# Kernel optimization log

Hardware: AMD Instinct MI355X
Metric: run time of the kernel (lower is better)

The kernel has to match this reference:

```python
import jax, jax.numpy as jnp
import numpy as np

EPS = 1e-6

def rms_norm(x):
    return x * jax.lax.rsqrt(jnp.mean(x * x, axis=-1, keepdims=True) + EPS)

def setup_inputs() -> dict:
    key = jax.random.key(0)
    k_x, k_w = jax.random.split(key)
    T, B, D = 2048, 16, 1024
    x = jax.random.normal(k_x, (T, B, D), dtype=jnp.float32)
    h0 = jnp.zeros((B, D), dtype=jnp.float32)
    # xavier_uniform for W: limit = sqrt(6/(fan_in+fan_out)) = sqrt(6/(2D))
    limit = float(np.sqrt(6.0 / (2 * D)))
    W = jax.random.uniform(k_w, (D, D), dtype=jnp.float32, minval=-limit, maxval=limit)
    b = jnp.zeros((D,), dtype=jnp.float32)
    log_alpha = jnp.asarray(np.log(0.1), dtype=jnp.float32)
    return {"x": x, "h0": h0, "W": W, "b": b, "log_alpha": log_alpha}

def reference(x, h0, W, b, log_alpha):
    # x: [T,B,D], h0: [B,D], W: [D,D], b: [D], log_alpha: []
    alpha = jnp.exp(log_alpha)
    # Precompute all input projections in one big GEMM: [T,B,D]
    Wx_all = jnp.einsum('tbd,ed->tbe', x, W) + b

    def step(h, wx):
        h_new = rms_norm(h + alpha * wx)
        out = h_new * jax.nn.silu(h_new)
        return h_new, (h_new, out)

    _, (hs, outs) = jax.lax.scan(step, h0, Wx_all)
    h = jnp.concatenate([h0[None], hs], axis=0)  # [T+1,B,D]
    return outs, h
```

## Files before the change

### kernel.cpp

```cpp
#include <hip/hip_runtime.h>
#include <hip/hip_bf16.h>

#define T_STEPS 2048
#define BATCH 16
#define DIM 1024
#define EPSV 1e-6f
#define INVD (1.0f / 1024.0f)
#define SLOTF (BATCH * DIM)
#define SLOT4C (BATCH * DIM / 4)

typedef short short8 __attribute__((ext_vector_type(8)));
typedef float f32x4 __attribute__((ext_vector_type(4)));

struct alignas(16) bf16x8pack { __hip_bfloat16 v[8]; };

__global__ __launch_bounds__(256) void cvt_kernel(const float* __restrict__ src,
                                                  bf16x8pack* __restrict__ dst, int n8) {
  int i = blockIdx.x * blockDim.x + threadIdx.x;
  if (i >= n8) return;
  const float4* s4 = (const float4*)src + (size_t)i * 2;
  float4 a = s4[0];
  float4 b = s4[1];
  bf16x8pack p;
  p.v[0] = __float2bfloat16(a.x); p.v[1] = __float2bfloat16(a.y);
  p.v[2] = __float2bfloat16(a.z); p.v[3] = __float2bfloat16(a.w);
  p.v[4] = __float2bfloat16(b.x); p.v[5] = __float2bfloat16(b.y);
  p.v[6] = __float2bfloat16(b.z); p.v[7] = __float2bfloat16(b.w);
  dst[i] = p;
}

__global__ __launch_bounds__(256) void gemm_kernel(
    const __hip_bfloat16* __restrict__ Xb,
    const __hip_bfloat16* __restrict__ Wb,
    const float* __restrict__ bias,
    const float* __restrict__ log_alpha_p,
    float* __restrict__ hreg) {
  __shared__ __hip_bfloat16 As[128 * 32];
  __shared__ __hip_bfloat16 Bs[128 * 32];
  const int tid = threadIdx.x;
  const int wave = tid >> 6, lane = tid & 63;
  const int m0 = blockIdx.y * 128;
  const int e0 = blockIdx.x * 128;
  const int wm = (wave >> 1) * 64;
  const int wn = (wave & 1) * 64;
  const int l15 = lane & 15, l4 = lane >> 4;

  f32x4 acc[4][4] = {};

  const int srow = wave * 16 + (lane >> 2);
  const int sch = (lane & 3) * 8;

  for (int kt = 0; kt < DIM; kt += 32) {
    __syncthreads();
#pragma unroll
    for (int i = 0; i < 2; ++i) {
      const __hip_bfloat16* ga = Xb + (size_t)(m0 + i * 64 + srow) * DIM + kt + sch;
      const __hip_bfloat16* gb = Wb + (size_t)(e0 + i * 64 + srow) * DIM + kt + sch;
      __builtin_amdgcn_global_load_lds(
          (const __attribute__((address_space(1))) void*)ga,
          (__attribute__((address_space(3))) void*)((char*)As + (i * 64 + wave * 16) * 64),
          16, 0, 0);
      __builtin_amdgcn_global_load_lds(
          (const __attribute__((address_space(1))) void*)gb,
          (__attribute__((address_space(3))) void*)((char*)Bs + (i * 64 + wave * 16) * 64),
          16, 0, 0);
    }
    __syncthreads();
    short8 a[4], b[4];
#pragma unroll
    for (int f = 0; f < 4; ++f)
      a[f] = *(const short8*)((const char*)As + ((wm + f * 16 + l15) * 32 + l4 * 8) * 2);
#pragma unroll
    for (int g = 0; g < 4; ++g)
      b[g] = *(const short8*)((const char*)Bs + ((wn + g * 16 + l15) * 32 + l4 * 8) * 2);
#pragma unroll
    for (int f = 0; f < 4; ++f)
#pragma unroll
      for (int g = 0; g < 4; ++g)
        acc[f][g] = __builtin_amdgcn_mfma_f32_16x16x32_bf16(a[f], b[g], acc[f][g], 0, 0, 0);
  }
  const float alpha = __expf(log_alpha_p[0]);
#pragma unroll
  for (int g = 0; g < 4; ++g) {
    const int e = e0 + wn + g * 16 + l15;
    const float bv = bias[e];
#pragma unroll
    for (int f = 0; f < 4; ++f) {
#pragma unroll
      for (int r = 0; r < 4; ++r) {
        const int m = m0 + wm + f * 16 + l4 * 4 + r;
        hreg[(size_t)(m + BATCH) * DIM + e] = alpha * (acc[f][g][r] + bv);
      }
    }
  }
}

__device__ __forceinline__ float dpp_sum_reg(float x) {
  float acc = x;
#define DPP_ADD(ctrl)                                                              \
  {                                                                                \
    int t_ = __builtin_amdgcn_update_dpp(0, __float_as_int(acc), (ctrl), 0xf, 0xf, \
                                         true);                                    \
    acc += __int_as_float(t_);                                                     \
  }
  DPP_ADD(0x111); DPP_ADD(0x112); DPP_ADD(0x114); DPP_ADD(0x118);
  DPP_ADD(0x142); DPP_ADD(0x143);
#undef DPP_ADD
  return acc;
}

__global__ __launch_bounds__(64) void dots_kernel(const float* __restrict__ hreg,
                                                  float4* __restrict__ scal4) {
  const int t = blockIdx.x >> 4;
  const int b = blockIdx.x & 15;
  const int lane = threadIdx.x;
  const float4* w  = (const float4*)(hreg + (size_t)(t + 1) * SLOTF + b * DIM);
  const float4* m1 = (const float4*)(hreg + (size_t)(t    ) * SLOTF + b * DIM);
  const float4* m2 = (const float4*)(hreg + (size_t)(t - 1) * SLOTF + b * DIM);
  const float4* m3 = (const float4*)(hreg + (size_t)(t - 2) * SLOTF + b * DIM);
  float e = 0.f, d = 0.f, d2 = 0.f, d3 = 0.f;
#pragma unroll
  for (int j = 0; j < 4; ++j) {
    float4 a = w[lane + 64 * j];
    e = fmaf(a.x, a.x, fmaf(a.y, a.y, fmaf(a.z, a.z, fmaf(a.w, a.w, e))));
    if (t >= 1) {
      float4 p = m1[lane + 64 * j];
      d = fmaf(p.x, a.x, fmaf(p.y, a.y, fmaf(p.z, a.z, fmaf(p.w, a.w, d))));
    }
    if (t >= 2) {
      float4 p = m2[lane + 64 * j];
      d2 = fmaf(p.x, a.x, fmaf(p.y, a.y, fmaf(p.z, a.z, fmaf(p.w, a.w, d2))));
    }
    if (t >= 3) {
      float4 p = m3[lane + 64 * j];
      d3 = fmaf(p.x, a.x, fmaf(p.y, a.y, fmaf(p.z, a.z, fmaf(p.w, a.w, d3))));
    }
  }
  e = dpp_sum_reg(e);
  d = dpp_sum_reg(d);
  d2 = dpp_sum_reg(d2);
  d3 = dpp_sum_reg(d3);
  if (lane == 63) scal4[b * T_STEPS + t] = make_float4(e, d, d2, d3);
}

__global__ __launch_bounds__(256) void scan_kernel(
    const float* __restrict__ h0,
    const float4* __restrict__ scal4,
    float* __restrict__ hreg) {
  const int b = blockIdx.x;
  const int tid = threadIdx.x;
  const int wave = tid >> 6;
  const int lane = tid & 63;
  float4* h4 = (float4*)hreg;
  const int idx4 = b * 256 + tid;

  __shared__ float4 scLDS[T_STEPS];
  __shared__ float Gp[4][4];
  __shared__ float initP[4][8];

#pragma unroll
  for (int p = 0; p < 8; ++p)
    scLDS[p * 256 + tid] = scal4[b * T_STEPS + p * 256 + tid];

  float4 w[8];
  w[2] = h4[(size_t)SLOT4C * 3 + idx4];
  w[3] = h4[(size_t)SLOT4C * 4 + idx4];
  w[4] = h4[(size_t)SLOT4C * 5 + idx4];
  w[5] = h4[(size_t)SLOT4C * 6 + idx4];
  w[6] = h4[(size_t)SLOT4C * 7 + idx4];
  w[7] = h4[(size_t)SLOT4C * 8 + idx4];
  w[0] = h4[(size_t)SLOT4C * 9 + idx4];
  w[1] = h4[(size_t)SLOT4C * 10 + idx4];
  float4 w0v = h4[(size_t)SLOT4C * 1 + idx4];
  float4 w1v = h4[(size_t)SLOT4C * 2 + idx4];
  float4 h0v = ((const float4*)h0)[idx4];
  h4[idx4] = h0v;

  float4 s;
  s.x = h0v.x + w0v.x; s.y = h0v.y + w0v.y;
  s.z = h0v.z + w0v.z; s.w = h0v.w + w0v.w;
  float q  = fmaf(s.x, s.x, fmaf(s.y, s.y, fmaf(s.z, s.z, s.w * s.w)));
  float r  = fmaf(s.x, w1v.x, fmaf(s.y, w1v.y, fmaf(s.z, w1v.z, s.w * w1v.w)));
  float u2 = fmaf(s.x, w[2].x, fmaf(s.y, w[2].y, fmaf(s.z, w[2].z, s.w * w[2].w)));
  float g3 = fmaf(h0v.x, w[3].x, fmaf(h0v.y, w[3].y, fmaf(h0v.z, w[3].z, h0v.w * w[3].w)));
  float u4 = fmaf(s.x, w[4].x, fmaf(s.y, w[4].y, fmaf(s.z, w[4].z, s.w * w[4].w)));
  q = dpp_sum_reg(q); r = dpp_sum_reg(r); u2 = dpp_sum_reg(u2);
  g3 = dpp_sum_reg(g3); u4 = dpp_sum_reg(u4);
  if (lane == 63) {
    initP[wave][0] = q; initP[wave][1] = r; initP[wave][2] = u2;
    initP[wave][3] = g3; initP[wave][4] = u4;
  }
  __syncthreads();
  const float n1  = initP[0][0] + initP[1][0] + initP[2][0] + initP[3][0];
  const float b1  = initP[0][1] + initP[1][1] + initP[2][1] + initP[3][1];
  const float c2  = initP[0][2] + initP[1][2] + initP[2][2] + initP[3][2];
  const float G3v = initP[0][3] + initP[1][3] + initP[2][3] + initP[3][3];
  const float c4  = initP[0][4] + initP[1][4] + initP[2][4] + initP[3][4];

  float4 sc0 = scLDS[2];
  float4 sc1 = scLDS[3];
  const float e1 = scLDS[1].x;

  const float rinv1 = rsqrtf(fmaf(n1, INVD, EPSV));
  float n = fmaf(rinv1, fmaf(rinv1, n1, 2.0f * b1), e1);
  const float b2p = fmaf(rinv1, c2, sc0.y);
  float gr1 = G3v;
  float gr0 = rinv1 * c4;

  {
    float4 hv;
    hv.x = rinv1 * s.x; hv.y = rinv1 * s.y; hv.z = rinv1 * s.z; hv.w = rinv1 * s.w;
    h4[(size_t)SLOT4C * 1 + idx4] = hv;
    s.x = hv.x + w1v.x; s.y = hv.y + w1v.y; s.z = hv.z + w1v.z; s.w = hv.w + w1v.w;
  }
  float rm1 = rinv1, rm2 = 0.0f;

#define STEP(IEXPR, WS, W3S, SCA, GPW, GPR, GRW, GRU, MODE)                          \
  {                                                                                  \
    const int i_ = (IEXPR);                                                          \
    const float rinv = rsqrtf(fmaf(n, INVD, EPSV));                                  \
    float bb;                                                                        \
    if ((MODE) == 1) bb = b2p;                                                       \
    else bb = fmaf(rm1, fmaf(rm2, SCA.w + GRU, SCA.z), SCA.y);                       \
    n = fmaf(rinv, fmaf(rinv, n, 2.0f * bb), SCA.x);                                 \
    float4 hv_;                                                                      \
    hv_.x = rinv * s.x; hv_.y = rinv * s.y;                                          \
    hv_.z = rinv * s.z; hv_.w = rinv * s.w;                                          \
    h4[(size_t)SLOT4C * i_ + idx4] = hv_;                                            \
    s.x = hv_.x + w[WS].x; s.y = hv_.y + w[WS].y;                                    \
    s.z = hv_.z + w[WS].z; s.w = hv_.w + w[WS].w;                                    \
    float p_ = fmaf(hv_.x, w[W3S].x, fmaf(hv_.y, w[W3S].y,                           \
               fmaf(hv_.z, w[W3S].z, hv_.w * w[W3S].w)));                            \
    p_ = dpp_sum_reg(p_);                                                            \
    if (lane == 63) Gp[GPW][wave] = p_;                                              \
    if ((MODE) == 0) {                                                               \
      float4 g4_ = *(const float4*)&Gp[GPR][0];                                      \
      GRW = (g4_.x + g4_.y) + (g4_.z + g4_.w);                                       \
    }                                                                                \
    const int ipf_ = (i_ + 8 < T_STEPS) ? i_ + 8 : T_STEPS - 1;                      \
    w[WS] = h4[(size_t)SLOT4C * (ipf_ + 1) + idx4];                                  \
    const int isc_ = (i_ + 2 < T_STEPS) ? i_ + 2 : T_STEPS - 1;                      \
    SCA = scLDS[isc_];                                                               \
    rm2 = rm1; rm1 = rinv;                                                           \
    asm volatile("s_waitcnt lgkmcnt(0)" ::: "memory");                               \
    __builtin_amdgcn_sched_barrier(0);                                               \
    __builtin_amdgcn_s_barrier();                                                    \
  }

  STEP(2, 2, 5, sc0, 2, 0, gr0, gr1, 1)
  STEP(3, 3, 6, sc1, 3, 0, gr0, gr1, 2)
  STEP(4, 4, 7, sc0, 0, 2, gr1, gr0, 0)

  for (int ii = 5; ii <= 2037; ii += 8) {
    STEP(ii + 0, 5, 0, sc1, 1, 3, gr0, gr1, 0)
    STEP(ii + 1, 6, 1, sc0, 2, 0, gr1, gr0, 0)
    STEP(ii + 2, 7, 2, sc1, 3, 1, gr0, gr1, 0)
    STEP(ii + 3, 0, 3, sc0, 0, 2, gr1, gr0, 0)
    STEP(ii + 4, 1, 4, sc1, 1, 3, gr0, gr1, 0)
    STEP(ii + 5, 2, 5, sc0, 2, 0, gr1, gr0, 0)
    STEP(ii + 6, 3, 6, sc1, 3, 1, gr0, gr1, 0)
    STEP(ii + 7, 4, 7, sc0, 0, 2, gr1, gr0, 0)
  }
  STEP(2045, 5, 0, sc1, 1, 3, gr0, gr1, 0)
  STEP(2046, 6, 1, sc0, 2, 0, gr1, gr0, 0)
  STEP(2047, 7, 2, sc1, 3, 1, gr0, gr1, 0)
#undef STEP

  const float rinvT = rsqrtf(fmaf(n, INVD, EPSV));
  float4 o;
  o.x = rinvT * s.x; o.y = rinvT * s.y; o.z = rinvT * s.z; o.w = rinvT * s.w;
  h4[(size_t)SLOT4C * T_STEPS + idx4] = o;
}

__global__ __launch_bounds__(256) void silu_kernel(const float4* __restrict__ hsrc,
                                                   float4* __restrict__ out4, int n4) {
  int i = blockIdx.x * blockDim.x + threadIdx.x;
  if (i >= n4) return;
  float4 h = hsrc[i];
  float4 o;
  o.x = h.x * h.x / (1.f + __expf(-h.x));
  o.y = h.y * h.y / (1.f + __expf(-h.y));
  o.z = h.z * h.z / (1.f + __expf(-h.z));
  o.w = h.w * h.w / (1.f + __expf(-h.w));
  out4[i] = o;
}

extern "C" void kernel_launch(void* const* d_in, const int* in_sizes, int n_in,
                              void* d_out, int out_size, void* d_ws, size_t ws_size,
                              hipStream_t stream) {
  (void)in_sizes; (void)n_in; (void)d_ws; (void)ws_size; (void)out_size;
  const float* x = (const float*)d_in[0];
  const float* h0 = (const float*)d_in[1];
  const float* W = (const float*)d_in[2];
  const float* bias = (const float*)d_in[3];
  const float* log_alpha = (const float*)d_in[4];

  float* out = (float*)d_out;
  float* hreg = out + (size_t)T_STEPS * BATCH * DIM;
  __hip_bfloat16* xb = (__hip_bfloat16*)d_out;
  __hip_bfloat16* wb = (__hip_bfloat16*)((char*)d_out + (size_t)T_STEPS * BATCH * DIM * 2);
  float4* scal4 = (float4*)(out + (size_t)26 * 1024 * 1024);

  const int nx8 = T_STEPS * BATCH * DIM / 8;
  const int nw8 = DIM * DIM / 8;
  cvt_kernel<<<nx8 / 256, 256, 0, stream>>>(x, (bf16x8pack*)xb, nx8);
  cvt_kernel<<<nw8 / 256, 256, 0, stream>>>(W, (bf16x8pack*)wb, nw8);

  dim3 ggrid(DIM / 128, (T_STEPS * BATCH) / 128);
  gemm_kernel<<<ggrid, 256, 0, stream>>>(xb, wb, bias, log_alpha, hreg);

  dots_kernel<<<T_STEPS * BATCH, 64, 0, stream>>>(hreg, scal4);

  scan_kernel<<<BATCH, 256, 0, stream>>>(h0, scal4, hreg);

  const int n4 = T_STEPS * BATCH * DIM / 4;
  silu_kernel<<<n4 / 256, 256, 0, stream>>>((const float4*)(hreg + BATCH * DIM),
                                            (float4*)out, n4);
}
```

Before: 609.3 us.

## Extend norm recurrence lookahead to four steps to relax per-step barrier latency

```diff
diff --git a/kernel.cpp b/kernel.cpp
--- a/kernel.cpp
+++ b/kernel.cpp
@@ -13,6 +13,10 @@
 typedef float f32x4 __attribute__((ext_vector_type(4)));
 
 struct alignas(16) bf16x8pack { __hip_bfloat16 v[8]; };
+
+__device__ __forceinline__ float dot4(const float4& a, const float4& c) {
+  return fmaf(a.x, c.x, fmaf(a.y, c.y, fmaf(a.z, c.z, a.w * c.w)));
+}
 
 __global__ __launch_bounds__(256) void cvt_kernel(const float* __restrict__ src,
                                                   bf16x8pack* __restrict__ dst, int n8) {
@@ -110,7 +114,8 @@
 }
 
 __global__ __launch_bounds__(64) void dots_kernel(const float* __restrict__ hreg,
-                                                  float4* __restrict__ scal4) {
+                                                  float4* __restrict__ scal4,
+                                                  float* __restrict__ d4g) {
   const int t = blockIdx.x >> 4;
   const int b = blockIdx.x & 15;
   const int lane = threadIdx.x;
@@ -118,34 +123,36 @@
   const float4* m1 = (const float4*)(hreg + (size_t)(t    ) * SLOTF + b * DIM);
   const float4* m2 = (const float4*)(hreg + (size_t)(t - 1) * SLOTF + b * DIM);
   const float4* m3 = (const float4*)(hreg + (size_t)(t - 2) * SLOTF + b * DIM);
-  float e = 0.f, d = 0.f, d2 = 0.f, d3 = 0.f;
+  const float4* m4 = (const float4*)(hreg + (size_t)(t - 3) * SLOTF + b * DIM);
+  float e = 0.f, d = 0.f, d2 = 0.f, d3 = 0.f, d4 = 0.f;
 #pragma unroll
   for (int j = 0; j < 4; ++j) {
     float4 a = w[lane + 64 * j];
     e = fmaf(a.x, a.x, fmaf(a.y, a.y, fmaf(a.z, a.z, fmaf(a.w, a.w, e))));
-    if (t >= 1) {
-      float4 p = m1[lane + 64 * j];
-      d = fmaf(p.x, a.x, fmaf(p.y, a.y, fmaf(p.z, a.z, fmaf(p.w, a.w, d))));
-    }
-    if (t >= 2) {
-      float4 p = m2[lane + 64 * j];
-      d2 = fmaf(p.x, a.x, fmaf(p.y, a.y, fmaf(p.z, a.z, fmaf(p.w, a.w, d2))));
-    }
-    if (t >= 3) {
-      float4 p = m3[lane + 64 * j];
-      d3 = fmaf(p.x, a.x, fmaf(p.y, a.y, fmaf(p.z, a.z, fmaf(p.w, a.w, d3))));
-    }
+    if (t >= 1) { float4 p = m1[lane + 64 * j];
+      d = fmaf(p.x, a.x, fmaf(p.y, a.y, fmaf(p.z, a.z, fmaf(p.w, a.w, d)))); }
+    if (t >= 2) { float4 p = m2[lane + 64 * j];
+      d2 = fmaf(p.x, a.x, fmaf(p.y, a.y, fmaf(p.z, a.z, fmaf(p.w, a.w, d2)))); }
+    if (t >= 3) { float4 p = m3[lane + 64 * j];
+      d3 = fmaf(p.x, a.x, fmaf(p.y, a.y, fmaf(p.z, a.z, fmaf(p.w, a.w, d3)))); }
+    if (t >= 4) { float4 p = m4[lane + 64 * j];
+      d4 = fmaf(p.x, a.x, fmaf(p.y, a.y, fmaf(p.z, a.z, fmaf(p.w, a.w, d4)))); }
   }
   e = dpp_sum_reg(e);
   d = dpp_sum_reg(d);
   d2 = dpp_sum_reg(d2);
   d3 = dpp_sum_reg(d3);
-  if (lane == 63) scal4[b * T_STEPS + t] = make_float4(e, d, d2, d3);
+  d4 = dpp_sum_reg(d4);
+  if (lane == 63) {
+    scal4[b * T_STEPS + t] = make_float4(e, d + d, d2 + d2, d3 + d3);
+    d4g[b * T_STEPS + t] = d4 + d4;
+  }
 }
 
 __global__ __launch_bounds__(256) void scan_kernel(
     const float* __restrict__ h0,
     const float4* __restrict__ scal4,
+    const float* __restrict__ d4g,
     float* __restrict__ hreg) {
   const int b = blockIdx.x;
   const int tid = threadIdx.x;
@@ -155,12 +162,16 @@
   const int idx4 = b * 256 + tid;
 
   __shared__ float4 scLDS[T_STEPS];
-  __shared__ float Gp[4][4];
+  __shared__ float d4LDS[T_STEPS];
+  __shared__ alignas(16) float Gp[4][4];
   __shared__ float initP[4][8];
 
 #pragma unroll
   for (int p = 0; p < 8; ++p)
     scLDS[p * 256 + tid] = scal4[b * T_STEPS + p * 256 + tid];
+#pragma unroll
+  for (int p = 0; p < 8; ++p)
+    d4LDS[p * 256 + tid] = d4g[b * T_STEPS + p * 256 + tid];
 
   float4 w[8];
   w[2] = h4[(size_t)SLOT4C * 3 + idx4];
@@ -179,91 +190,123 @@
   float4 s;
   s.x = h0v.x + w0v.x; s.y = h0v.y + w0v.y;
   s.z = h0v.z + w0v.z; s.w = h0v.w + w0v.w;
-  float q  = fmaf(s.x, s.x, fmaf(s.y, s.y, fmaf(s.z, s.z, s.w * s.w)));
-  float r  = fmaf(s.x, w1v.x, fmaf(s.y, w1v.y, fmaf(s.z, w1v.z, s.w * w1v.w)));
-  float u2 = fmaf(s.x, w[2].x, fmaf(s.y, w[2].y, fmaf(s.z, w[2].z, s.w * w[2].w)));
-  float g3 = fmaf(h0v.x, w[3].x, fmaf(h0v.y, w[3].y, fmaf(h0v.z, w[3].z, h0v.w * w[3].w)));
-  float u4 = fmaf(s.x, w[4].x, fmaf(s.y, w[4].y, fmaf(s.z, w[4].z, s.w * w[4].w)));
-  q = dpp_sum_reg(q); r = dpp_sum_reg(r); u2 = dpp_sum_reg(u2);
-  g3 = dpp_sum_reg(g3); u4 = dpp_sum_reg(u4);
+  float q = dpp_sum_reg(dot4(s, s));
+  float r = dpp_sum_reg(dot4(s, w1v));
+  float u2 = dpp_sum_reg(dot4(s, w[2]));
+  float u3 = dpp_sum_reg(dot4(s, w[3]));
+  float g4 = dpp_sum_reg(dot4(h0v, w[4]));
   if (lane == 63) {
     initP[wave][0] = q; initP[wave][1] = r; initP[wave][2] = u2;
-    initP[wave][3] = g3; initP[wave][4] = u4;
+    initP[wave][3] = g4; initP[wave][4] = u3;
   }
   __syncthreads();
-  const float n1  = initP[0][0] + initP[1][0] + initP[2][0] + initP[3][0];
-  const float b1  = initP[0][1] + initP[1][1] + initP[2][1] + initP[3][1];
-  const float c2  = initP[0][2] + initP[1][2] + initP[2][2] + initP[3][2];
-  const float G3v = initP[0][3] + initP[1][3] + initP[2][3] + initP[3][3];
-  const float c4  = initP[0][4] + initP[1][4] + initP[2][4] + initP[3][4];
-
-  float4 sc0 = scLDS[2];
-  float4 sc1 = scLDS[3];
+  const float n1 = (initP[0][0] + initP[1][0]) + (initP[2][0] + initP[3][0]);
+  float bs = (initP[0][1] + initP[1][1]) + (initP[2][1] + initP[3][1]);
+  float c2s = (initP[0][2] + initP[1][2]) + (initP[2][2] + initP[3][2]);
+  float g4s = (initP[0][3] + initP[1][3]) + (initP[2][3] + initP[3][3]);
+  float c3s = (initP[0][4] + initP[1][4]) + (initP[2][4] + initP[3][4]);
+  const float B1 = bs + bs;
+  const float C2 = c2s + c2s;
+  const float C3 = c3s + c3s;
+  float gr0 = g4s + g4s;
+  float gr1 = 0.0f;
+
   const float e1 = scLDS[1].x;
-
-  const float rinv1 = rsqrtf(fmaf(n1, INVD, EPSV));
-  float n = fmaf(rinv1, fmaf(rinv1, n1, 2.0f * b1), e1);
-  const float b2p = fmaf(rinv1, c2, sc0.y);
-  float gr1 = G3v;
-  float gr0 = rinv1 * c4;
+  float4 sc2 = scLDS[2], sc3 = scLDS[3];
+  float4 scA = scLDS[4], scB = scLDS[5];
+  float d4A = d4LDS[4], d4B = d4LDS[5];
+  float4 rv = make_float4(0.f, 0.f, 0.f, 0.f);
+  float n = n1, rm1, rm2, rm3, pp;
 
   {
+    const float rinv = rsqrtf(fmaf(n, INVD, EPSV));
+    n = fmaf(rinv, fmaf(rinv, n, B1), e1);
     float4 hv;
-    hv.x = rinv1 * s.x; hv.y = rinv1 * s.y; hv.z = rinv1 * s.z; hv.w = rinv1 * s.w;
+    hv.x = rinv * s.x; hv.y = rinv * s.y; hv.z = rinv * s.z; hv.w = rinv * s.w;
     h4[(size_t)SLOT4C * 1 + idx4] = hv;
     s.x = hv.x + w1v.x; s.y = hv.y + w1v.y; s.z = hv.z + w1v.z; s.w = hv.w + w1v.w;
-  }
-  float rm1 = rinv1, rm2 = 0.0f;
-
-#define STEP(IEXPR, WS, W3S, SCA, GPW, GPR, GRW, GRU, MODE)                          \
+    pp = dpp_sum_reg(dot4(hv, w[5]));
+    rm1 = rinv;
+    asm volatile("s_waitcnt lgkmcnt(0)" ::: "memory");
+    __builtin_amdgcn_s_barrier();
+  }
+  {
+    if (lane == 63) Gp[1][wave] = pp;
+    const float rinv = rsqrtf(fmaf(n, INVD, EPSV));
+    const float BB = fmaf(rm1, C2, sc2.y);
+    n = fmaf(rinv, fmaf(rinv, n, BB), sc2.x);
+    float4 hv;
+    hv.x = rinv * s.x; hv.y = rinv * s.y; hv.z = rinv * s.z; hv.w = rinv * s.w;
+    h4[(size_t)SLOT4C * 2 + idx4] = hv;
+    s.x = hv.x + w[2].x; s.y = hv.y + w[2].y; s.z = hv.z + w[2].z; s.w = hv.w + w[2].w;
+    pp = dpp_sum_reg(dot4(hv, w[6]));
+    w[2] = h4[(size_t)SLOT4C * 11 + idx4];
+    rm2 = rm1; rm1 = rinv;
+    asm volatile("s_waitcnt lgkmcnt(0)" ::: "memory");
+    __builtin_amdgcn_s_barrier();
+  }
+  {
+    if (lane == 63) Gp[2][wave] = pp;
+    const float rinv = rsqrtf(fmaf(n, INVD, EPSV));
+    const float BB = fmaf(rm1, fmaf(rm2, C3, sc3.z), sc3.y);
+    n = fmaf(rinv, fmaf(rinv, n, BB), sc3.x);
+    rv = *(const float4*)&Gp[1][0];
+    float4 hv;
+    hv.x = rinv * s.x; hv.y = rinv * s.y; hv.z = rinv * s.z; hv.w = rinv * s.w;
+    h4[(size_t)SLOT4C * 3 + idx4] = hv;
+    s.x = hv.x + w[3].x; s.y = hv.y + w[3].y; s.z = hv.z + w[3].z; s.w = hv.w + w[3].w;
+    pp = dpp_sum_reg(dot4(hv, w[7]));
+    w[3] = h4[(size_t)SLOT4C * 12 + idx4];
+    rm3 = rm2; rm2 = rm1; rm1 = rinv;
+    asm volatile("s_waitcnt lgkmcnt(0)" ::: "memory");
+    __builtin_amdgcn_s_barrier();
+  }
+
+#define STEP(I_, WS, W4S, GW, GR, SC, D4R, GRU, GRW)                                 \
   {                                                                                  \
-    const int i_ = (IEXPR);                                                          \
+    const int i_ = (I_);                                                             \
+    if (lane == 63) Gp[GW][wave] = pp;                                               \
+    asm volatile("" ::: "memory");                                                   \
     const float rinv = rsqrtf(fmaf(n, INVD, EPSV));                                  \
-    float bb;                                                                        \
-    if ((MODE) == 1) bb = b2p;                                                       \
-    else bb = fmaf(rm1, fmaf(rm2, SCA.w + GRU, SCA.z), SCA.y);                       \
-    n = fmaf(rinv, fmaf(rinv, n, 2.0f * bb), SCA.x);                                 \
+    const float BB =                                                                 \
+        fmaf(rm1, fmaf(rm2, fmaf(rm3, (D4R) + (GRU), (SC).w), (SC).z), (SC).y);      \
+    n = fmaf(rinv, fmaf(rinv, n, BB), (SC).x);                                       \
+    {                                                                                \
+      float gt_ = (rv.x + rv.y) + (rv.z + rv.w);                                     \
+      GRW = gt_ + gt_;                                                               \
+    }                                                                                \
+    rv = *(const float4*)&Gp[GR][0];                                                 \
+    const int isc_ = (i_ + 2 < T_STEPS) ? (i_ + 2) : (T_STEPS - 1);                  \
+    SC = scLDS[isc_];                                                                \
+    D4R = d4LDS[isc_];                                                               \
     float4 hv_;                                                                      \
     hv_.x = rinv * s.x; hv_.y = rinv * s.y;                                          \
     hv_.z = rinv * s.z; hv_.w = rinv * s.w;                                          \
     h4[(size_t)SLOT4C * i_ + idx4] = hv_;                                            \
     s.x = hv_.x + w[WS].x; s.y = hv_.y + w[WS].y;                                    \
     s.z = hv_.z + w[WS].z; s.w = hv_.w + w[WS].w;                                    \
-    float p_ = fmaf(hv_.x, w[W3S].x, fmaf(hv_.y, w[W3S].y,                           \
-               fmaf(hv_.z, w[W3S].z, hv_.w * w[W3S].w)));                            \
-    p_ = dpp_sum_reg(p_);                                                            \
-    if (lane == 63) Gp[GPW][wave] = p_;                                              \
-    if ((MODE) == 0) {                                                               \
-      float4 g4_ = *(const float4*)&Gp[GPR][0];                                      \
-      GRW = (g4_.x + g4_.y) + (g4_.z + g4_.w);                                       \
-    }                                                                                \
-    const int ipf_ = (i_ + 8 < T_STEPS) ? i_ + 8 : T_STEPS - 1;                      \
+    pp = dpp_sum_reg(dot4(hv_, w[W4S]));                                             \
+    const int ipf_ = (i_ + 8 < T_STEPS) ? (i_ + 8) : (T_STEPS - 1);                  \
     w[WS] = h4[(size_t)SLOT4C * (ipf_ + 1) + idx4];                                  \
-    const int isc_ = (i_ + 2 < T_STEPS) ? i_ + 2 : T_STEPS - 1;                      \
-    SCA = scLDS[isc_];                                                               \
-    rm2 = rm1; rm1 = rinv;                                                           \
-    asm volatile("s_waitcnt lgkmcnt(0)" ::: "memory");                               \
-    __builtin_amdgcn_sched_barrier(0);                                               \
+    rm3 = rm2; rm2 = rm1; rm1 = rinv;                                                \
+    asm volatile("s_waitcnt lgkmcnt(3)" ::: "memory");                               \
     __builtin_amdgcn_s_barrier();                                                    \
   }
 
-  STEP(2, 2, 5, sc0, 2, 0, gr0, gr1, 1)
-  STEP(3, 3, 6, sc1, 3, 0, gr0, gr1, 2)
-  STEP(4, 4, 7, sc0, 0, 2, gr1, gr0, 0)
-
-  for (int ii = 5; ii <= 2037; ii += 8) {
-    STEP(ii + 0, 5, 0, sc1, 1, 3, gr0, gr1, 0)
-    STEP(ii + 1, 6, 1, sc0, 2, 0, gr1, gr0, 0)
-    STEP(ii + 2, 7, 2, sc1, 3, 1, gr0, gr1, 0)
-    STEP(ii + 3, 0, 3, sc0, 0, 2, gr1, gr0, 0)
-    STEP(ii + 4, 1, 4, sc1, 1, 3, gr0, gr1, 0)
-    STEP(ii + 5, 2, 5, sc0, 2, 0, gr1, gr0, 0)
-    STEP(ii + 6, 3, 6, sc1, 3, 1, gr0, gr1, 0)
-    STEP(ii + 7, 4, 7, sc0, 0, 2, gr1, gr0, 0)
-  }
-  STEP(2045, 5, 0, sc1, 1, 3, gr0, gr1, 0)
-  STEP(2046, 6, 1, sc0, 2, 0, gr1, gr0, 0)
-  STEP(2047, 7, 2, sc1, 3, 1, gr0, gr1, 0)
+  for (int ii = 4; ii <= 2036; ii += 8) {
+    STEP(ii + 0, 4, 0, 3, 2, scA, d4A, gr0, gr1)
+    STEP(ii + 1, 5, 1, 0, 3, scB, d4B, gr1, gr0)
+    STEP(ii + 2, 6, 2, 1, 0, scA, d4A, gr0, gr1)
+    STEP(ii + 3, 7, 3, 2, 1, scB, d4B, gr1, gr0)
+    STEP(ii + 4, 0, 4, 3, 2, scA, d4A, gr0, gr1)
+    STEP(ii + 5, 1, 5, 0, 3, scB, d4B, gr1, gr0)
+    STEP(ii + 6, 2, 6, 1, 0, scA, d4A, gr0, gr1)
+    STEP(ii + 7, 3, 7, 2, 1, scB, d4B, gr1, gr0)
+  }
+  STEP(2044, 4, 0, 3, 2, scA, d4A, gr0, gr1)
+  STEP(2045, 5, 1, 0, 3, scB, d4B, gr1, gr0)
+  STEP(2046, 6, 2, 1, 0, scA, d4A, gr0, gr1)
+  STEP(2047, 7, 3, 2, 1, scB, d4B, gr1, gr0)
 #undef STEP
 
   const float rinvT = rsqrtf(fmaf(n, INVD, EPSV));
@@ -300,6 +343,7 @@
   __hip_bfloat16* xb = (__hip_bfloat16*)d_out;
   __hip_bfloat16* wb = (__hip_bfloat16*)((char*)d_out + (size_t)T_STEPS * BATCH * DIM * 2);
   float4* scal4 = (float4*)(out + (size_t)26 * 1024 * 1024);
+  float* d4g = out + (size_t)27 * 1024 * 1024;
 
   const int nx8 = T_STEPS * BATCH * DIM / 8;
   const int nw8 = DIM * DIM / 8;
@@ -309,9 +353,9 @@
   dim3 ggrid(DIM / 128, (T_STEPS * BATCH) / 128);
   gemm_kernel<<<ggrid, 256, 0, stream>>>(xb, wb, bias, log_alpha, hreg);
 
-  dots_kernel<<<T_STEPS * BATCH, 64, 0, stream>>>(hreg, scal4);
-
-  scan_kernel<<<BATCH, 256, 0, stream>>>(h0, scal4, hreg);
+  dots_kernel<<<T_STEPS * BATCH, 64, 0, stream>>>(hreg, scal4, d4g);
+
+  scan_kernel<<<BATCH, 256, 0, stream>>>(h0, scal4, d4g, hreg);
 
   const int n4 = T_STEPS * BATCH * DIM / 4;
   silu_kernel<<<n4 / 256, 256, 0, stream>>>((const float4*)(hreg + BATCH * DIM),
```

Measured after the change: 592.4 us. 2.8% less time.
